# Kernel tuning notes

Measured on AMD Instinct MI355X. Metric: run time of the kernel, lower is better.

Reference implementation:

```python
import jax, jax.numpy as jnp
import numpy as np

N = 50000      # nodes (B*N flattened)
E = 800000     # edges
IN = 128       # in_channels
HID = 32       # hidden_channels per head
HEADS = 2
OUT = 64       # out_channels
NEG_SLOPE = 0.2


def setup_inputs() -> dict:
    key = jax.random.key(0)
    ks = jax.random.split(key, 10)
    x = jax.random.normal(ks[0], (N, IN), jnp.float32)
    edge_index = jax.random.randint(ks[1], (2, E), 0, N, dtype=jnp.int64)
    s = 0.1
    W1 = jax.random.normal(ks[2], (IN, HEADS * HID), jnp.float32) * s
    a_src1 = jax.random.normal(ks[3], (HEADS, HID), jnp.float32) * s
    a_dst1 = jax.random.normal(ks[4], (HEADS, HID), jnp.float32) * s
    b1 = jnp.zeros((HEADS * HID,), jnp.float32)
    W2 = jax.random.normal(ks[5], (HEADS * HID, OUT), jnp.float32) * s
    a_src2 = jax.random.normal(ks[6], (1, OUT), jnp.float32) * s
    a_dst2 = jax.random.normal(ks[7], (1, OUT), jnp.float32) * s
    b2 = jnp.zeros((OUT,), jnp.float32)
    return {"x": x, "edge_index": edge_index,
            "W1": W1, "a_src1": a_src1, "a_dst1": a_dst1, "b1": b1,
            "W2": W2, "a_src2": a_src2, "a_dst2": a_dst2, "b2": b2}


def gat_conv(x, src, dst, W, a_s, a_d, b, heads, ch, concat):
    """PyG GATConv: per-edge attention, softmax over incoming edges of dst."""
    n = x.shape[0]
    h = (x @ W).reshape(n, heads, ch)                       # [N,H,C]
    al_s = (h * a_s).sum(-1)                                # [N,H]
    al_d = (h * a_d).sum(-1)                                # [N,H]
    e = jax.nn.leaky_relu(al_s[src] + al_d[dst], NEG_SLOPE)  # [E,H]
    e_max = jax.ops.segment_max(e, dst, num_segments=n)     # [N,H]
    ex = jnp.exp(e - e_max[dst])
    denom = jax.ops.segment_sum(ex, dst, num_segments=n)
    coef = ex / (denom[dst] + 1e-16)                         # [E,H]
    out = jax.ops.segment_sum(h[src] * coef[:, :, None], dst, num_segments=n)  # [N,H,C]
    out = out.reshape(n, heads * ch) if concat else out.mean(axis=1)
    return out + b


def reference(x, edge_index, W1, a_src1, a_dst1, b1, W2, a_src2, a_dst2, b2):
    loops = jnp.arange(N, dtype=edge_index.dtype)
    src = jnp.concatenate([edge_index[0], loops])  # add_self_loops=True (PyG default)
    dst = jnp.concatenate([edge_index[1], loops])
    h1 = jax.nn.relu(gat_conv(x, src, dst, W1, a_src1, a_dst1, b1, HEADS, HID, True))
    return gat_conv(h1, src, dst, W2, a_src2, a_dst2, b2, 1, OUT, False)
```

## Files before the change

### kernel.cpp

```cpp
#include <hip/hip_runtime.h>

#define IN_CH   128
#define HIDX    64
#define NEG_SLOPE 0.2f
#define CAP     64

static inline size_t align256(size_t x) { return (x + 255) & ~(size_t)255; }

__global__ void k_build(const int* __restrict__ ei, int E, int N,
                        int* __restrict__ cnt, int* __restrict__ csrf) {
    int i = blockIdx.x * blockDim.x + threadIdx.x;
    int ET = E + N;
    if (i >= ET) return;
    int s, d;
    if (i < E) { s = ei[i]; d = ei[E + i]; }
    else       { s = i - E; d = i - E; }
    int r = atomicAdd(&cnt[d], 1);
    if (r < CAP) csrf[(size_t)d * CAP + r] = s;
}

template <int K, int H, bool RELU_IN>
__global__ __launch_bounds__(256)
void k_gemm(const float* __restrict__ X, const float* __restrict__ W,
            const float* __restrict__ bin,
            const float* __restrict__ a_s, const float* __restrict__ a_d,
            float* __restrict__ Hout, float* __restrict__ als,
            float* __restrict__ ald, int N) {
    constexpr int STR = 68;
    __shared__ float Wl[K * 64];
    __shared__ float xT[K * STR];

    const int t  = threadIdx.x;
    const int nb = blockIdx.x * 64;

    {
        const float4* W4 = (const float4*)W;
        float4* Wl4 = (float4*)Wl;
#pragma unroll
        for (int i = 0; i < (K * 16) / 256; ++i)
            Wl4[i * 256 + t] = W4[i * 256 + t];
    }
    {
        constexpr int QK = K / 4;
        constexpr int RS = 256 / QK;
        const int kq = t % QK;
        const int r0 = t / QK;
        for (int n = r0; n < 64; n += RS) {
            const int node = nb + n;
            const int cn = node < N ? node : N - 1;
            float4 v = *(const float4*)(X + (size_t)cn * K + kq * 4);
            if (RELU_IN) {
                const float4 bv = *(const float4*)(bin + kq * 4);
                v.x = fmaxf(v.x + bv.x, 0.f);
                v.y = fmaxf(v.y + bv.y, 0.f);
                v.z = fmaxf(v.z + bv.z, 0.f);
                v.w = fmaxf(v.w + bv.w, 0.f);
            }
            const int ns = (((n >> 2) ^ (kq & 7)) << 2) + (n & 3);
            xT[(kq * 4 + 0) * STR + ns] = v.x;
            xT[(kq * 4 + 1) * STR + ns] = v.y;
            xT[(kq * 4 + 2) * STR + ns] = v.z;
            xT[(kq * 4 + 3) * STR + ns] = v.w;
        }
    }
    __syncthreads();

    const int cg = t & 15;
    const int ng = t >> 4;

    float acc[4][4] = {{0.f}};
#pragma unroll 4
    for (int k = 0; k < K; ++k) {
        const int xb = ((ng ^ ((k >> 2) & 7)) << 2);
        const float4 xv = *(const float4*)&xT[k * STR + xb];
        const float4 wv = *(const float4*)&Wl[k * 64 + (cg << 2)];
        acc[0][0] += xv.x * wv.x; acc[0][1] += xv.x * wv.y;
        acc[0][2] += xv.x * wv.z; acc[0][3] += xv.x * wv.w;
        acc[1][0] += xv.y * wv.x; acc[1][1] += xv.y * wv.y;
        acc[1][2] += xv.y * wv.z; acc[1][3] += xv.y * wv.w;
        acc[2][0] += xv.z * wv.x; acc[2][1] += xv.z * wv.y;
        acc[2][2] += xv.z * wv.z; acc[2][3] += xv.z * wv.w;
        acc[3][0] += xv.w * wv.x; acc[3][1] += xv.w * wv.y;
        acc[3][2] += xv.w * wv.z; acc[3][3] += xv.w * wv.w;
    }

    const float4 asv = *(const float4*)(a_s + cg * 4);
    const float4 adv = *(const float4*)(a_d + cg * 4);
#pragma unroll
    for (int i = 0; i < 4; ++i) {
        const int node = nb + ng * 4 + i;
        float ps = acc[i][0] * asv.x + acc[i][1] * asv.y +
                   acc[i][2] * asv.z + acc[i][3] * asv.w;
        float pd = acc[i][0] * adv.x + acc[i][1] * adv.y +
                   acc[i][2] * adv.z + acc[i][3] * adv.w;
#pragma unroll
        for (int m = 1; m < (H == 2 ? 8 : 16); m <<= 1) {
            ps += __shfl_xor(ps, m, 64);
            pd += __shfl_xor(pd, m, 64);
        }
        if (node < N) {
            *(float4*)(Hout + (size_t)node * 64 + cg * 4) =
                make_float4(acc[i][0], acc[i][1], acc[i][2], acc[i][3]);
            if (H == 2) {
                if ((cg & 7) == 0) {
                    als[node * 2 + (cg >> 3)] = ps;
                    ald[node * 2 + (cg >> 3)] = pd;
                }
            } else if (cg == 0) {
                als[node] = ps;
                ald[node] = pd;
            }
        }
    }
}

template <int H>
__global__ __launch_bounds__(256)
void k_agg(const int* __restrict__ cnt, const int* __restrict__ csrf,
           const float* __restrict__ als, const float* __restrict__ ald,
           const float* __restrict__ h, const float* __restrict__ bias,
           float* __restrict__ out, int N) {
    int wid = blockIdx.x * 4 + (threadIdx.x >> 6);
    int lane = threadIdx.x & 63;
    if (wid >= N) return;

    int deg = cnt[wid]; if (deg > CAP) deg = CAP;
    const int g  = lane >> 4;
    const int cl = lane & 15;
    const int head = (H == 2) ? (cl >> 3) : 0;
    const float aldh = ald[wid * H + head];
    const size_t base = (size_t)wid * CAP;

    float4 acc = make_float4(0.f, 0.f, 0.f, 0.f);
    float dsum = 0.f;
#pragma unroll 2
    for (int j = g; j < deg; j += 4) {
        const int s = csrf[base + j];
        float e = als[s * H + head] + aldh;
        e = e > 0.f ? e : NEG_SLOPE * e;
        const float c = __expf(e);
        dsum += c;
        const float4 hv = *(const float4*)(h + (size_t)s * 64 + cl * 4);
        acc.x += c * hv.x; acc.y += c * hv.y;
        acc.z += c * hv.z; acc.w += c * hv.w;
    }
#pragma unroll
    for (int m = 16; m < 64; m <<= 1) {
        acc.x += __shfl_xor(acc.x, m, 64);
        acc.y += __shfl_xor(acc.y, m, 64);
        acc.z += __shfl_xor(acc.z, m, 64);
        acc.w += __shfl_xor(acc.w, m, 64);
        dsum  += __shfl_xor(dsum,  m, 64);
    }
    if (g == 0) {
        const float inv = 1.0f / (dsum + 1e-16f);
        float4 r;
        if (bias) {
            const float4 bv = *(const float4*)(bias + cl * 4);
            r = make_float4(acc.x * inv + bv.x, acc.y * inv + bv.y,
                            acc.z * inv + bv.z, acc.w * inv + bv.w);
        } else {
            r = make_float4(acc.x * inv, acc.y * inv, acc.z * inv, acc.w * inv);
        }
        *(float4*)(out + (size_t)wid * 64 + cl * 4) = r;
    }
}

extern "C" void kernel_launch(void* const* d_in, const int* in_sizes, int n_in,
                              void* d_out, int out_size, void* d_ws, size_t ws_size,
                              hipStream_t stream) {
    const float* x   = (const float*)d_in[0];
    const int*   ei  = (const int*)d_in[1];
    const float* W1  = (const float*)d_in[2];
    const float* as1 = (const float*)d_in[3];
    const float* ad1 = (const float*)d_in[4];
    const float* b1  = (const float*)d_in[5];
    const float* W2  = (const float*)d_in[6];
    const float* as2 = (const float*)d_in[7];
    const float* ad2 = (const float*)d_in[8];
    const float* b2  = (const float*)d_in[9];
    float* out = (float*)d_out;

    const int N  = in_sizes[0] / IN_CH;
    const int E  = in_sizes[1] / 2;
    const int ET = E + N;

    char* ws = (char*)d_ws;
    size_t o = 0;
    auto alloc = [&](size_t bytes) { void* p = ws + o; o = align256(o + bytes); return p; };
    int*   cnt  = (int*)alloc((size_t)N * sizeof(int));
    int*   csrf = (int*)alloc((size_t)N * CAP * sizeof(int));
    float* h    = (float*)alloc((size_t)N * 64 * sizeof(float));
    float* als1 = (float*)alloc((size_t)N * 2 * sizeof(float));
    float* ald1 = (float*)alloc((size_t)N * 2 * sizeof(float));
    float* als2 = (float*)alloc((size_t)N * sizeof(float));
    float* ald2 = (float*)alloc((size_t)N * sizeof(float));
    float* out1 = out;

    hipMemsetAsync(cnt, 0, (size_t)N * sizeof(int), stream);
    k_build<<<(ET + 255) / 256, 256, 0, stream>>>(ei, E, N, cnt, csrf);

    const int gg = (N + 63) / 64;
    const int gn = (N + 3) / 4;

    k_gemm<IN_CH, 2, false><<<gg, 256, 0, stream>>>(x, W1, nullptr, as1, ad1,
                                                    h, als1, ald1, N);
    k_agg<2><<<gn, 256, 0, stream>>>(cnt, csrf, als1, ald1, h, nullptr, out1, N);

    k_gemm<HIDX, 1, true><<<gg, 256, 0, stream>>>(out1, W2, b1, as2, ad2,
                                                  h, als2, ald2, N);
    k_agg<1><<<gn, 256, 0, stream>>>(cnt, csrf, als2, ald2, h, b2, out, N);
}
```

Baseline: 168.0 us.

## Build adjacency via two-pass bucketing with shared-memory atomics

```diff
diff --git a/kernel.cpp b/kernel.cpp
--- a/kernel.cpp
+++ b/kernel.cpp
@@ -4,19 +4,54 @@
 #define HIDX    64
 #define NEG_SLOPE 0.2f
 #define CAP     64
+#define BNODES  128
+#define NSEG    4
+#define SEGCAP  1024
 
 static inline size_t align256(size_t x) { return (x + 255) & ~(size_t)255; }
 
-__global__ void k_build(const int* __restrict__ ei, int E, int N,
-                        int* __restrict__ cnt, int* __restrict__ csrf) {
+__global__ void k_bucket(const int* __restrict__ ei, int E, int N,
+                         int* __restrict__ bcnt, unsigned* __restrict__ bkt) {
     int i = blockIdx.x * blockDim.x + threadIdx.x;
     int ET = E + N;
     if (i >= ET) return;
     int s, d;
     if (i < E) { s = ei[i]; d = ei[E + i]; }
     else       { s = i - E; d = i - E; }
-    int r = atomicAdd(&cnt[d], 1);
-    if (r < CAP) csrf[(size_t)d * CAP + r] = s;
+    const int slot = (d >> 7) * NSEG + (i & (NSEG - 1));
+    int pos = atomicAdd(&bcnt[slot], 1);
+    if (pos < SEGCAP)
+        bkt[(size_t)slot * SEGCAP + pos] =
+            ((unsigned)(d & (BNODES - 1)) << 16) | (unsigned)s;
+}
+
+__global__ __launch_bounds__(256)
+void k_fill(const int* __restrict__ bcnt, const unsigned* __restrict__ bkt,
+            int N, int* __restrict__ cnt, int* __restrict__ csrf) {
+    __shared__ int lcnt[BNODES];
+    const int b = blockIdx.x;
+    const int t = threadIdx.x;
+    if (t < BNODES) lcnt[t] = 0;
+    __syncthreads();
+    const int nb = b * BNODES;
+#pragma unroll
+    for (int seg = 0; seg < NSEG; ++seg) {
+        int m = bcnt[b * NSEG + seg];
+        if (m > SEGCAP) m = SEGCAP;
+        const unsigned* src = bkt + (size_t)(b * NSEG + seg) * SEGCAP;
+        for (int i = t; i < m; i += 256) {
+            const unsigned v = src[i];
+            const int dl = v >> 16;
+            const int s  = v & 0xFFFF;
+            const int r  = atomicAdd(&lcnt[dl], 1);
+            if (r < CAP) csrf[(size_t)(nb + dl) * CAP + r] = s;
+        }
+    }
+    __syncthreads();
+    if (t < BNODES && nb + t < N) {
+        const int c = lcnt[t];
+        cnt[nb + t] = c < CAP ? c : CAP;
+    }
 }
 
 template <int K, int H, bool RELU_IN>
@@ -124,7 +159,7 @@
     int lane = threadIdx.x & 63;
     if (wid >= N) return;
 
-    int deg = cnt[wid]; if (deg > CAP) deg = CAP;
+    const int deg = cnt[wid];
     const int g  = lane >> 4;
     const int cl = lane & 15;
     const int head = (H == 2) ? (cl >> 3) : 0;
@@ -181,24 +216,29 @@
     const float* b2  = (const float*)d_in[9];
     float* out = (float*)d_out;
 
-    const int N  = in_sizes[0] / IN_CH;
-    const int E  = in_sizes[1] / 2;
-    const int ET = E + N;
+    const int N    = in_sizes[0] / IN_CH;
+    const int E    = in_sizes[1] / 2;
+    const int ET   = E + N;
+    const int NBUK = (N + BNODES - 1) / BNODES;
 
     char* ws = (char*)d_ws;
     size_t o = 0;
     auto alloc = [&](size_t bytes) { void* p = ws + o; o = align256(o + bytes); return p; };
-    int*   cnt  = (int*)alloc((size_t)N * sizeof(int));
-    int*   csrf = (int*)alloc((size_t)N * CAP * sizeof(int));
-    float* h    = (float*)alloc((size_t)N * 64 * sizeof(float));
-    float* als1 = (float*)alloc((size_t)N * 2 * sizeof(float));
-    float* ald1 = (float*)alloc((size_t)N * 2 * sizeof(float));
-    float* als2 = (float*)alloc((size_t)N * sizeof(float));
-    float* ald2 = (float*)alloc((size_t)N * sizeof(float));
-    float* out1 = out;
-
-    hipMemsetAsync(cnt, 0, (size_t)N * sizeof(int), stream);
-    k_build<<<(ET + 255) / 256, 256, 0, stream>>>(ei, E, N, cnt, csrf);
+    int*      cnt  = (int*)alloc((size_t)N * sizeof(int));
+    int*      bcnt = (int*)alloc((size_t)NBUK * NSEG * sizeof(int));
+    unsigned* bkt  = (unsigned*)alloc((size_t)NBUK * NSEG * SEGCAP * sizeof(unsigned));
+    int*      csrf = (int*)alloc((size_t)N * CAP * sizeof(int));
+    float*    h    = (float*)alloc((size_t)N * 64 * sizeof(float));
+    float*    als1 = (float*)alloc((size_t)N * 2 * sizeof(float));
+    float*    ald1 = (float*)alloc((size_t)N * 2 * sizeof(float));
+    float*    als2 = (float*)alloc((size_t)N * sizeof(float));
+    float*    ald2 = (float*)alloc((size_t)N * sizeof(float));
+    float*    out1 = out;
+
+    hipMemsetAsync(bcnt, 0, (size_t)NBUK * NSEG * sizeof(int), stream);
+
+    k_bucket<<<(ET + 255) / 256, 256, 0, stream>>>(ei, E, N, bcnt, bkt);
+    k_fill<<<NBUK, 256, 0, stream>>>(bcnt, bkt, N, cnt, csrf);
 
     const int gg = (N + 63) / 64;
     const int gn = (N + 3) / 4;
```

Result: slower. 243.2 us (+44.7%).
